# Kernel tuning notes

Hardware: AMD Instinct MI355X
Metric: run time of the kernel (lower is better)

The kernel has to match this reference:

```python
import jax, jax.numpy as jnp
import numpy as np

N = 100000      # nodes
E = 1600000     # edges (avg degree 16)
IN_DIM = 256
HID = 128
EPS = 0.3


def setup_inputs() -> dict:
    key = jax.random.key(0)
    ks = jax.random.split(key, 6)
    x = jax.random.normal(ks[0], (N, IN_DIM), dtype=jnp.float32)
    # edges without self-loops (dst = src + nonzero offset mod N)
    src = jax.random.randint(ks[1], (E,), 0, N)
    off = jax.random.randint(ks[2], (E,), 1, N)
    dst = (src + off) % N
    edge_index = jnp.stack([src, dst]).astype(jnp.int32)
    # xavier_normal_ with gain=1.414 for t1 and gate
    g1 = 1.414 * np.sqrt(2.0 / (IN_DIM + HID))
    w1 = (jax.random.normal(ks[3], (HID, IN_DIM)) * g1).astype(jnp.float32)
    b1 = jnp.zeros((HID,), jnp.float32)
    gg = 1.414 * np.sqrt(2.0 / (2 * HID + 1))
    gate_w = (jax.random.normal(ks[4], (1, 2 * HID)) * gg).astype(jnp.float32)
    gate_b = jnp.zeros((1,), jnp.float32)
    return dict(x=x, edge_index=edge_index, w1=w1, b1=b1, gate_w=gate_w, gate_b=gate_b)


def reference(x, edge_index, w1, b1, gate_w, gate_b):
    src, dst = edge_index[0], edge_index[1]
    # in-degree based symmetric norm, deg clamped to >= 1
    deg = jax.ops.segment_sum(jnp.ones((E,), jnp.float32), dst, num_segments=N)
    norm = jnp.clip(deg, 1.0) ** -0.5  # [N]

    h = jax.nn.relu(x @ w1.T + b1)     # [N, HID] (dropout p=0 / eval -> identity)
    raw = h

    # gate([h_dst, h_src]) decomposed: concat @ W^T = h_dst @ w_d + h_src @ w_s
    w_d, w_s = gate_w[0, :HID], gate_w[0, HID:]
    a_dst = h @ w_d                    # [N]
    a_src = h @ w_s                    # [N]
    g = jnp.tanh(a_dst[dst] + a_src[src] + gate_b[0])   # [E] per-edge gate
    e = g * norm[dst] * norm[src]                        # [E]

    # u_mul_e + sum: gather src features, weight, scatter-add to dst
    z = jax.ops.segment_sum(h[src] * e[:, None], dst, num_segments=N)  # [N, HID]
    return EPS * raw + z
```

## Files before the change

### kernel.cpp

```cpp
#include <hip/hip_runtime.h>
#include <math.h>
#include <stdint.h>

#define N_NODES 100000
#define N_EDGES 1600000
#define IN_DIM  256
#define HID     128
#define EPS_C   0.3f

#define NPB      128
#define NBKT     782
#define NBKT_P   784
#define BCAP     3072
#define S1_CHUNK 4096
#define S1_BLOCKS 391
#define GC(b)    ((b) * 16)

#define PK_SRC(p)  ((p) & 0x1FFFF)
#define PK_LI(p)   ((p) >> 17)

typedef __attribute__((ext_vector_type(8))) __bf16 bf16x8;
typedef __attribute__((ext_vector_type(4))) float  f32x4;
typedef __attribute__((ext_vector_type(8))) unsigned short ushort8;

static __device__ __forceinline__ unsigned short f2bf(float f) {
    unsigned u = __float_as_uint(f);
    unsigned r = (u + 0x7fffu + ((u >> 16) & 1u)) >> 16;
    return (unsigned short)r;
}
static __device__ __forceinline__ float bf2f(unsigned short s) {
    return __uint_as_float((unsigned)s << 16);
}
static __device__ __forceinline__ float fast_tanh(float x) {
    float e = __builtin_exp2f(x * 2.8853900817779268f);
    return 1.0f - 2.0f / (e + 1.0f);
}

__global__ __launch_bounds__(256) void convert_w1_kernel(const float* __restrict__ w1,
                                                         unsigned short* __restrict__ w1b) {
    int i = blockIdx.x * 256 + threadIdx.x;
    if (i * 4 >= HID * IN_DIM) return;
    float4 v = *(const float4*)&w1[i * 4];
    ushort4 r;
    r.x = f2bf(v.x); r.y = f2bf(v.y); r.z = f2bf(v.z); r.w = f2bf(v.w);
    *(ushort4*)&w1b[i * 4] = r;
}

__global__ __launch_bounds__(512) void partition_kernel(const int* __restrict__ src,
                                                        const int* __restrict__ dst,
                                                        int* __restrict__ gcur,
                                                        int* __restrict__ ebuf) {
    __shared__ int hist[NBKT_P];
    __shared__ int cur[NBKT_P];

    int t = threadIdx.x;
    for (int i = t; i < NBKT_P; i += 512) hist[i] = 0;
    __syncthreads();

    int base4 = blockIdx.x * (S1_CHUNK / 4);
    int rem4  = N_EDGES / 4 - base4;

    int4 sv[2], dv[2];
#pragma unroll
    for (int j = 0; j < 2; j++) {
        int i4 = j * 512 + t;
        if (i4 < rem4) {
            sv[j] = *(const int4*)&src[(base4 + i4) * 4];
            dv[j] = *(const int4*)&dst[(base4 + i4) * 4];
        } else {
            dv[j] = make_int4(-1, -1, -1, -1);
        }
    }
#pragma unroll
    for (int j = 0; j < 2; j++) {
        if (dv[j].x >= 0) {
            atomicAdd(&hist[dv[j].x >> 7], 1);
            atomicAdd(&hist[dv[j].y >> 7], 1);
            atomicAdd(&hist[dv[j].z >> 7], 1);
            atomicAdd(&hist[dv[j].w >> 7], 1);
        }
    }
    __syncthreads();

    if (t < NBKT_P / 2) {
        int h0 = hist[2 * t], h1 = hist[2 * t + 1];
        if (h0 > 0) cur[2 * t]     = atomicAdd(&gcur[GC(2 * t)], h0);
        if (h1 > 0) cur[2 * t + 1] = atomicAdd(&gcur[GC(2 * t + 1)], h1);
    }
    __syncthreads();

#pragma unroll
    for (int j = 0; j < 2; j++) {
        if (dv[j].x >= 0) {
            int b, p;
            b = dv[j].x >> 7; p = atomicAdd(&cur[b], 1);
            if (p < BCAP) ebuf[(size_t)b * BCAP + p] = ((dv[j].x & (NPB - 1)) << 17) | sv[j].x;
            b = dv[j].y >> 7; p = atomicAdd(&cur[b], 1);
            if (p < BCAP) ebuf[(size_t)b * BCAP + p] = ((dv[j].y & (NPB - 1)) << 17) | sv[j].y;
            b = dv[j].z >> 7; p = atomicAdd(&cur[b], 1);
            if (p < BCAP) ebuf[(size_t)b * BCAP + p] = ((dv[j].z & (NPB - 1)) << 17) | sv[j].z;
            b = dv[j].w >> 7; p = atomicAdd(&cur[b], 1);
            if (p < BCAP) ebuf[(size_t)b * BCAP + p] = ((dv[j].w & (NPB - 1)) << 17) | sv[j].w;
        }
    }
}

__global__ __launch_bounds__(512) void deg_kernel(const int* __restrict__ gcur,
                                                  const int* __restrict__ ebuf,
                                                  int2* __restrict__ rs2,
                                                  float* __restrict__ nrm) {
    __shared__ int dcnt[NPB];
    __shared__ int s[NPB];
    int b = blockIdx.x;
    int t = threadIdx.x;
    if (t < NPB) dcnt[t] = 0;
    __syncthreads();

    int ecnt = gcur[GC(b)];
    if (ecnt > BCAP) ecnt = BCAP;
    for (int j = t; j < ecnt; j += 512)
        atomicAdd(&dcnt[PK_LI(ebuf[(size_t)b * BCAP + j])], 1);
    __syncthreads();

    int v = 0;
    if (t < NPB) { v = dcnt[t]; s[t] = v; }
    __syncthreads();
    for (int off = 1; off < NPB; off <<= 1) {
        int a = (t < NPB && t >= off) ? s[t - off] : 0;
        __syncthreads();
        if (t < NPB) s[t] += a;
        __syncthreads();
    }

    int nbase = b * NPB;
    int nn = N_NODES - nbase;
    if (nn > NPB) nn = NPB;
    if (t < nn) {
        int incl = s[t];
        rs2[nbase + t] = make_int2(b * BCAP + incl - v, b * BCAP + incl);
        nrm[nbase + t] = rsqrtf(fmaxf((float)v, 1.0f));
    }
}

__global__ __launch_bounds__(256) void gemm_kernel(const float* __restrict__ x,
                                                   const unsigned short* __restrict__ w1b,
                                                   const float* __restrict__ b1,
                                                   const float* __restrict__ gw,
                                                   const float* __restrict__ nrm,
                                                   unsigned short* __restrict__ h,
                                                   float2* __restrict__ pd_pack,
                                                   float2* __restrict__ ps_pack) {
    int tid  = threadIdx.x;
    int bm   = blockIdx.x * 64;
    int wv   = tid >> 6;
    int lane = tid & 63;
    int col  = lane & 15;
    int kq   = lane >> 4;

    int row  = bm + wv * 16 + col;
    bool rok = row < N_NODES;
    const float* ap = &x[(size_t)row * IN_DIM + kq * 8];

    bf16x8 af[8];
#pragma unroll
    for (int i = 0; i < 8; i++) {
        float4 a0 = {0, 0, 0, 0}, a1 = {0, 0, 0, 0};
        if (rok) {
            a0 = *(const float4*)(ap + 32 * i);
            a1 = *(const float4*)(ap + 32 * i + 4);
        }
        ushort8 av;
        av[0] = f2bf(a0.x); av[1] = f2bf(a0.y); av[2] = f2bf(a0.z); av[3] = f2bf(a0.w);
        av[4] = f2bf(a1.x); av[5] = f2bf(a1.y); av[6] = f2bf(a1.z); av[7] = f2bf(a1.w);
        af[i] = *(bf16x8*)&av;
    }

    f32x4 acc[8];
#pragma unroll
    for (int nf = 0; nf < 8; nf++) acc[nf] = (f32x4){0.f, 0.f, 0.f, 0.f};

#pragma unroll
    for (int i = 0; i < 8; i++) {
#pragma unroll
        for (int nf = 0; nf < 8; nf++) {
            bf16x8 bfrag = *(const bf16x8*)&w1b[(nf * 16 + col) * IN_DIM + i * 32 + kq * 8];
            acc[nf] = __builtin_amdgcn_mfma_f32_16x16x32_bf16(af[i], bfrag, acc[nf], 0, 0, 0);
        }
    }

    float bias[8], wd[8], wsv[8];
#pragma unroll
    for (int nf = 0; nf < 8; nf++) {
        bias[nf] = b1[nf * 16 + col];
        wd[nf]   = gw[nf * 16 + col];
        wsv[nf]  = gw[HID + nf * 16 + col];
    }
#pragma unroll
    for (int r = 0; r < 4; r++) {
        int gm = bm + wv * 16 + kq * 4 + r;
        float pd = 0.f, ps = 0.f;
        bool ok = (gm < N_NODES);
#pragma unroll
        for (int nf = 0; nf < 8; nf++) {
            float v = fmaxf(acc[nf][r] + bias[nf], 0.f);
            pd = fmaf(v, wd[nf], pd);
            ps = fmaf(v, wsv[nf], ps);
            if (ok) h[(size_t)gm * HID + nf * 16 + col] = f2bf(v);
        }
#pragma unroll
        for (int m = 1; m < 16; m <<= 1) {
            pd += __shfl_xor(pd, m);
            ps += __shfl_xor(ps, m);
        }
        if (ok && col == 0) {
            float nv = nrm[gm];
            pd_pack[gm] = make_float2(pd, nv);
            ps_pack[gm] = make_float2(ps, nv);
        }
    }
}

__global__ __launch_bounds__(1024) void spagg2_kernel(const int* __restrict__ gcur,
                                                      const int* __restrict__ ebuf,
                                                      const int2* __restrict__ rs2,
                                                      const float2* __restrict__ pd_pack,
                                                      const float2* __restrict__ ps_pack,
                                                      const float* __restrict__ gb,
                                                      const unsigned short* __restrict__ h,
                                                      float* __restrict__ out) {
    __shared__ int2   sorted[BCAP];
    __shared__ int    curs[NPB];
    __shared__ int    begs[NPB];
    __shared__ int    ends[NPB];
    __shared__ float2 pdl[NPB];

    int b = blockIdx.x;
    int t = threadIdx.x;
    int nbase = b * NPB;

    if (t < NPB) {
        int node = nbase + t;
        if (node < N_NODES) {
            int2 r = rs2[node];
            int lb = r.x - b * BCAP;
            begs[t] = lb; curs[t] = lb;
            ends[t] = r.y - b * BCAP;
            pdl[t]  = pd_pack[node];
        } else {
            begs[t] = 0; curs[t] = 0; ends[t] = 0;
            pdl[t] = make_float2(0.f, 0.f);
        }
    }
    __syncthreads();

    int ecnt = gcur[GC(b)];
    if (ecnt > BCAP) ecnt = BCAP;
    float gbv = gb[0];

    for (int j = t; j < ecnt; j += 1024) {
        int p  = ebuf[(size_t)b * BCAP + j];
        int s  = PK_SRC(p);
        int li = PK_LI(p);
        int pos = atomicAdd(&curs[li], 1);
        float2 pdp = pdl[li];
        float2 psp = ps_pack[s];
        float g = fast_tanh(pdp.x + psp.x + gbv) * pdp.y * psp.y;
        sorted[pos] = make_int2(s, __float_as_int(g));
    }
    __syncthreads();

    int lane = t & 63;
    int w    = t >> 6;
    int q  = lane >> 4;
    int ql = lane & 15;

#pragma unroll
    for (int k = 0; k < NPB / 16; k++) {
        int li = w + 16 * k;
        int node = nbase + li;
        if (node >= N_NODES) continue;
        int beg = begs[li];
        int end = ends[li];

        float acc[8];
#pragma unroll
        for (int u = 0; u < 8; u++) acc[u] = 0.f;

        int j = beg;
        for (; j + 8 <= end; j += 8) {
            int2 e0 = sorted[j + q];
            int2 e1 = sorted[j + 4 + q];
            ushort8 r0 = *(const ushort8*)&h[(size_t)e0.x * HID + ql * 8];
            ushort8 r1 = *(const ushort8*)&h[(size_t)e1.x * HID + ql * 8];
            float c0 = __int_as_float(e0.y);
            float c1 = __int_as_float(e1.y);
#pragma unroll
            for (int u = 0; u < 8; u++) {
                acc[u] = fmaf(c0, bf2f(r0[u]), acc[u]);
                acc[u] = fmaf(c1, bf2f(r1[u]), acc[u]);
            }
        }
        for (; j < end; j += 4) {
            bool act = (j + q) < end;
            int idx = act ? (j + q) : beg;
            int2 e = sorted[idx];
            ushort8 r = *(const ushort8*)&h[(size_t)e.x * HID + ql * 8];
            float c = act ? __int_as_float(e.y) : 0.f;
#pragma unroll
            for (int u = 0; u < 8; u++) acc[u] = fmaf(c, bf2f(r[u]), acc[u]);
        }
#pragma unroll
        for (int u = 0; u < 8; u++) {
            acc[u] += __shfl_xor(acc[u], 16);
            acc[u] += __shfl_xor(acc[u], 32);
        }
        if (q == 0) {
            ushort8 hd = *(const ushort8*)&h[(size_t)node * HID + ql * 8];
            f32x4 o0, o1;
            o0.x = fmaf(EPS_C, bf2f(hd[0]), acc[0]);
            o0.y = fmaf(EPS_C, bf2f(hd[1]), acc[1]);
            o0.z = fmaf(EPS_C, bf2f(hd[2]), acc[2]);
            o0.w = fmaf(EPS_C, bf2f(hd[3]), acc[3]);
            o1.x = fmaf(EPS_C, bf2f(hd[4]), acc[4]);
            o1.y = fmaf(EPS_C, bf2f(hd[5]), acc[5]);
            o1.z = fmaf(EPS_C, bf2f(hd[6]), acc[6]);
            o1.w = fmaf(EPS_C, bf2f(hd[7]), acc[7]);
            __builtin_nontemporal_store(o0, (f32x4*)&out[(size_t)node * HID + ql * 8]);
            __builtin_nontemporal_store(o1, (f32x4*)&out[(size_t)node * HID + ql * 8 + 4]);
        }
    }
}

extern "C" void kernel_launch(void* const* d_in, const int* in_sizes, int n_in,
                              void* d_out, int out_size, void* d_ws, size_t ws_size,
                              hipStream_t stream) {
    const float* x  = (const float*)d_in[0];
    const int*   ei = (const int*)d_in[1];
    const float* w1 = (const float*)d_in[2];
    const float* b1 = (const float*)d_in[3];
    const float* gw = (const float*)d_in[4];
    const float* gb = (const float*)d_in[5];
    float* out = (float*)d_out;

    const int* src = ei;
    const int* dst = ei + N_EDGES;

    uintptr_t base = (uintptr_t)d_ws;
    size_t off = 0;
    auto alloc = [&](size_t bytes) -> void* {
        void* p = (void*)(base + off);
        off += (bytes + 255) & ~(size_t)255;
        return p;
    };
    unsigned short* h   = (unsigned short*)alloc((size_t)N_NODES * HID * 2);
    float2* pd_pack     = (float2*)alloc((size_t)N_NODES * 8);
    float2* ps_pack     = (float2*)alloc((size_t)N_NODES * 8);
    float*  nrm         = (float*)alloc((size_t)N_NODES * 4);
    int2*   rs2         = (int2*)alloc((size_t)N_NODES * 8);
    unsigned short* w1b = (unsigned short*)alloc((size_t)HID * IN_DIM * 2);
    int*    gcur        = (int*)alloc((size_t)NBKT * 16 * 4);
    int*    ebuf        = (int*)alloc((size_t)NBKT * BCAP * 4);

    (void)hipMemsetAsync(gcur, 0, (size_t)NBKT * 16 * 4, stream);

    convert_w1_kernel<<<(HID * IN_DIM / 4 + 255) / 256, 256, 0, stream>>>(w1, w1b);
    partition_kernel<<<S1_BLOCKS, 512, 0, stream>>>(src, dst, gcur, ebuf);
    deg_kernel<<<NBKT, 512, 0, stream>>>(gcur, ebuf, rs2, nrm);
    gemm_kernel<<<(N_NODES + 63) / 64, 256, 0, stream>>>(x, w1b, b1, gw, nrm,
                                                         h, pd_pack, ps_pack);
    spagg2_kernel<<<NBKT, 1024, 0, stream>>>(gcur, ebuf, rs2,
                                             pd_pack, ps_pack, gb, h, out);
}
```

Measured before the change: 337.6 us.

## Stage partition writes in LDS, widen buckets, and cache W1 in LDS for GEMM

The partition kernel now doubles bucket width to 256 nodes and chunk size to 8192 edges. It sorts each chunk's edges into bucket-contiguous order in shared memory through a prefix scan, then writes them to global memory in coalesced runs, finding each element's bucket by binary search. The GEMM kernel now uses 512-thread blocks of 128 rows and copies the bf16 W1 into XOR-swizzled LDS so the B fragments come from shared memory rather than global or L2. Risks are fewer blocks in partition and the spmm stage, heavier LDS use limiting occupancy, and whether unseen kernels such as deg and spagg handle NPB=256 correctly.

New measurement: 287.8 us. 1.17x faster.

```diff
diff --git a/kernel.cpp b/kernel.cpp
--- a/kernel.cpp
+++ b/kernel.cpp
@@ -8,12 +8,11 @@
 #define HID     128
 #define EPS_C   0.3f
 
-#define NPB      128
-#define NBKT     782
-#define NBKT_P   784
-#define BCAP     3072
-#define S1_CHUNK 4096
-#define S1_BLOCKS 391
+#define NPB      256
+#define NBKT     391
+#define BCAP     5504
+#define S1_CHUNK 8192
+#define S1_BLOCKS 196
 #define GC(b)    ((b) * 16)
 
 #define PK_SRC(p)  ((p) & 0x1FFFF)
@@ -50,19 +49,23 @@
                                                         const int* __restrict__ dst,
                                                         int* __restrict__ gcur,
                                                         int* __restrict__ ebuf) {
-    __shared__ int hist[NBKT_P];
-    __shared__ int cur[NBKT_P];
+    __shared__ int hist[NBKT];
+    __shared__ int base[NBKT];
+    __shared__ int gpos[NBKT];
+    __shared__ int cur[NBKT];
+    __shared__ int seg[512];
+    __shared__ int staged[S1_CHUNK];
 
     int t = threadIdx.x;
-    for (int i = t; i < NBKT_P; i += 512) hist[i] = 0;
+    if (t < NBKT) hist[t] = 0;
     __syncthreads();
 
     int base4 = blockIdx.x * (S1_CHUNK / 4);
     int rem4  = N_EDGES / 4 - base4;
 
-    int4 sv[2], dv[2];
-#pragma unroll
-    for (int j = 0; j < 2; j++) {
+    int4 sv[4], dv[4];
+#pragma unroll
+    for (int j = 0; j < 4; j++) {
         int i4 = j * 512 + t;
         if (i4 < rem4) {
             sv[j] = *(const int4*)&src[(base4 + i4) * 4];
@@ -72,36 +75,59 @@
         }
     }
 #pragma unroll
-    for (int j = 0; j < 2; j++) {
+    for (int j = 0; j < 4; j++) {
         if (dv[j].x >= 0) {
-            atomicAdd(&hist[dv[j].x >> 7], 1);
-            atomicAdd(&hist[dv[j].y >> 7], 1);
-            atomicAdd(&hist[dv[j].z >> 7], 1);
-            atomicAdd(&hist[dv[j].w >> 7], 1);
-        }
-    }
-    __syncthreads();
-
-    if (t < NBKT_P / 2) {
-        int h0 = hist[2 * t], h1 = hist[2 * t + 1];
-        if (h0 > 0) cur[2 * t]     = atomicAdd(&gcur[GC(2 * t)], h0);
-        if (h1 > 0) cur[2 * t + 1] = atomicAdd(&gcur[GC(2 * t + 1)], h1);
-    }
-    __syncthreads();
-
-#pragma unroll
-    for (int j = 0; j < 2; j++) {
+            atomicAdd(&hist[dv[j].x >> 8], 1);
+            atomicAdd(&hist[dv[j].y >> 8], 1);
+            atomicAdd(&hist[dv[j].z >> 8], 1);
+            atomicAdd(&hist[dv[j].w >> 8], 1);
+        }
+    }
+    __syncthreads();
+
+    seg[t] = (t < NBKT) ? hist[t] : 0;
+    __syncthreads();
+    for (int off = 1; off < 512; off <<= 1) {
+        int a = (t >= off) ? seg[t - off] : 0;
+        __syncthreads();
+        seg[t] += a;
+        __syncthreads();
+    }
+    if (t < NBKT) {
+        int excl = seg[t] - hist[t];
+        base[t] = excl;
+        cur[t]  = excl;
+        if (hist[t] > 0) gpos[t] = atomicAdd(&gcur[GC(t)], hist[t]);
+    }
+    __syncthreads();
+
+#pragma unroll
+    for (int j = 0; j < 4; j++) {
         if (dv[j].x >= 0) {
             int b, p;
-            b = dv[j].x >> 7; p = atomicAdd(&cur[b], 1);
-            if (p < BCAP) ebuf[(size_t)b * BCAP + p] = ((dv[j].x & (NPB - 1)) << 17) | sv[j].x;
-            b = dv[j].y >> 7; p = atomicAdd(&cur[b], 1);
-            if (p < BCAP) ebuf[(size_t)b * BCAP + p] = ((dv[j].y & (NPB - 1)) << 17) | sv[j].y;
-            b = dv[j].z >> 7; p = atomicAdd(&cur[b], 1);
-            if (p < BCAP) ebuf[(size_t)b * BCAP + p] = ((dv[j].z & (NPB - 1)) << 17) | sv[j].z;
-            b = dv[j].w >> 7; p = atomicAdd(&cur[b], 1);
-            if (p < BCAP) ebuf[(size_t)b * BCAP + p] = ((dv[j].w & (NPB - 1)) << 17) | sv[j].w;
-        }
+            b = dv[j].x >> 8; p = atomicAdd(&cur[b], 1);
+            staged[p] = ((dv[j].x & (NPB - 1)) << 17) | sv[j].x;
+            b = dv[j].y >> 8; p = atomicAdd(&cur[b], 1);
+            staged[p] = ((dv[j].y & (NPB - 1)) << 17) | sv[j].y;
+            b = dv[j].z >> 8; p = atomicAdd(&cur[b], 1);
+            staged[p] = ((dv[j].z & (NPB - 1)) << 17) | sv[j].z;
+            b = dv[j].w >> 8; p = atomicAdd(&cur[b], 1);
+            staged[p] = ((dv[j].w & (NPB - 1)) << 17) | sv[j].w;
+        }
+    }
+    __syncthreads();
+
+    int n = N_EDGES - base4 * 4;
+    if (n > S1_CHUNK) n = S1_CHUNK;
+    for (int i = t; i < n; i += 512) {
+        int w = staged[i];
+        int lo = 0, hi = NBKT - 1;
+        while (lo < hi) {
+            int mid = (lo + hi + 1) >> 1;
+            if (base[mid] <= i) lo = mid; else hi = mid - 1;
+        }
+        int off2 = gpos[lo] + (i - base[lo]);
+        if (off2 < BCAP) ebuf[(size_t)lo * BCAP + off2] = w;
     }
 }
 
@@ -142,20 +168,38 @@
     }
 }
 
-__global__ __launch_bounds__(256) void gemm_kernel(const float* __restrict__ x,
-                                                   const unsigned short* __restrict__ w1b,
-                                                   const float* __restrict__ b1,
-                                                   const float* __restrict__ gw,
-                                                   const float* __restrict__ nrm,
-                                                   unsigned short* __restrict__ h,
-                                                   float2* __restrict__ pd_pack,
-                                                   float2* __restrict__ ps_pack) {
+__global__ __launch_bounds__(512, 4) void gemm_kernel(const float* __restrict__ x,
+                                                      const unsigned short* __restrict__ w1b,
+                                                      const float* __restrict__ b1,
+                                                      const float* __restrict__ gw,
+                                                      const float* __restrict__ nrm,
+                                                      unsigned short* __restrict__ h,
+                                                      float2* __restrict__ pd_pack,
+                                                      float2* __restrict__ ps_pack) {
+    __shared__ unsigned short Bs[HID * IN_DIM];
+
     int tid  = threadIdx.x;
-    int bm   = blockIdx.x * 64;
+    int bm   = blockIdx.x * 128;
     int wv   = tid >> 6;
     int lane = tid & 63;
     int col  = lane & 15;
     int kq   = lane >> 4;
+
+    {
+        int n  = tid >> 2;
+        int c0 = tid & 3;
+        const unsigned short* srcp = &w1b[n * IN_DIM];
+#pragma unroll
+        for (int j = 0; j < 8; j++) {
+            int c = c0 + 4 * j;
+            *(ushort8*)((char*)Bs + n * 512 + ((c ^ (n & 7)) * 16)) =
+                *(const ushort8*)&srcp[c * 8];
+        }
+    }
+
+    f32x4 acc[8];
+#pragma unroll
+    for (int nf = 0; nf < 8; nf++) acc[nf] = (f32x4){0.f, 0.f, 0.f, 0.f};
 
     int row  = bm + wv * 16 + col;
     bool rok = row < N_NODES;
@@ -175,15 +219,15 @@
         af[i] = *(bf16x8*)&av;
     }
 
-    f32x4 acc[8];
-#pragma unroll
-    for (int nf = 0; nf < 8; nf++) acc[nf] = (f32x4){0.f, 0.f, 0.f, 0.f};
+    __syncthreads();
 
 #pragma unroll
     for (int i = 0; i < 8; i++) {
+        int swz = (4 * i + kq) ^ (col & 7);
 #pragma unroll
         for (int nf = 0; nf < 8; nf++) {
-            bf16x8 bfrag = *(const bf16x8*)&w1b[(nf * 16 + col) * IN_DIM + i * 32 + kq * 8];
+            int n = nf * 16 + col;
+            bf16x8 bfrag = *(bf16x8*)((char*)Bs + n * 512 + swz * 16);
             acc[nf] = __builtin_amdgcn_mfma_f32_16x16x32_bf16(af[i], bfrag, acc[nf], 0, 0, 0);
         }
     }
@@ -366,8 +410,8 @@
     convert_w1_kernel<<<(HID * IN_DIM / 4 + 255) / 256, 256, 0, stream>>>(w1, w1b);
     partition_kernel<<<S1_BLOCKS, 512, 0, stream>>>(src, dst, gcur, ebuf);
     deg_kernel<<<NBKT, 512, 0, stream>>>(gcur, ebuf, rs2, nrm);
-    gemm_kernel<<<(N_NODES + 63) / 64, 256, 0, stream>>>(x, w1b, b1, gw, nrm,
-                                                         h, pd_pack, ps_pack);
+    gemm_kernel<<<(N_NODES + 127) / 128, 512, 0, stream>>>(x, w1b, b1, gw, nrm,
+                                                           h, pd_pack, ps_pack);
     spagg2_kernel<<<NBKT, 1024, 0, stream>>>(gcur, ebuf, rs2,
                                              pd_pack, ps_pack, gb, h, out);
 }
```
